# Kernel optimization log

Measured on AMD Instinct MI355X. Metric: run time of the kernel, lower is better.

## Reference

```python
import jax, jax.numpy as jnp
import numpy as np

E = 512        # emb_size
H = 2 * E      # LSTM units
B = 512        # beam/query batch (batched Python-loop states)
K = 32         # padded candidates per state
T = 8          # max_path_length
N_ENT = 50000
N_REL = 5000


def setup_inputs() -> dict:
    key = jax.random.key(0)
    ks = jax.random.split(key, 12)
    f32 = jnp.float32
    ent_emb = jax.random.normal(ks[0], (N_ENT, E), f32) * 0.05
    rel_emb = jax.random.normal(ks[1], (N_REL, E), f32) * 0.05
    relation = jax.random.normal(ks[2], (B, E), f32) * 0.05
    Wx = jax.random.normal(ks[3], (H, 4 * H), f32) * 0.02
    Wh = jax.random.normal(ks[4], (H, 4 * H), f32) * 0.02
    b = jnp.zeros((4 * H,), f32)
    W1 = jax.random.normal(ks[5], (4 * E, 3 * E), f32) * 0.02
    b1 = jnp.zeros((3 * E,), f32)
    W2 = jax.random.normal(ks[6], (3 * E, 2 * E), f32) * 0.02
    b2 = jnp.zeros((2 * E,), f32)
    current_ids = jax.random.randint(ks[7], (T, B), 0, N_ENT)
    prev_rel_ids = jax.random.randint(ks[8], (T, B), 0, N_REL)
    cand_rel_ids = jax.random.randint(ks[9], (T, B, K), 0, N_REL)
    cand_ent_ids = jax.random.randint(ks[10], (T, B, K), 0, N_ENT)
    return {
        "ent_emb": ent_emb, "rel_emb": rel_emb, "relation": relation,
        "Wx": Wx, "Wh": Wh, "b": b,
        "W1": W1, "b1": b1, "W2": W2, "b2": b2,
        "current_ids": current_ids, "prev_rel_ids": prev_rel_ids,
        "cand_rel_ids": cand_rel_ids, "cand_ent_ids": cand_ent_ids,
    }


def reference(ent_emb, rel_emb, relation, Wx, Wh, b, W1, b1, W2, b2,
              current_ids, prev_rel_ids, cand_rel_ids, cand_ent_ids):
    Bh = relation.shape[0]
    units = Wh.shape[0]
    h0 = jnp.zeros((Bh, units), ent_emb.dtype)
    c0 = jnp.zeros((Bh, units), ent_emb.dtype)

    def step(carry, xs):
        h, c = carry
        cur, prl, crel, cent = xs
        # LSTMCell input: concat(prev relation vec, current entity vec)  [B, 2E]
        x = jnp.concatenate([rel_emb[prl], ent_emb[cur]], axis=-1)
        z = x @ Wx + h @ Wh + b                      # [B, 4H], keras gate order i,f,g,o
        i_, f_, g_, o_ = jnp.split(z, 4, axis=-1)
        c = jax.nn.sigmoid(f_) * c + jax.nn.sigmoid(i_) * jnp.tanh(g_)
        h = jax.nn.sigmoid(o_) * jnp.tanh(c)
        # posterior MLP on concat(ent, history, relation)  [B, 4E] -> [B, 2E]
        feat = jax.nn.relu(jnp.concatenate([ent_emb[cur], h, relation], axis=-1) @ W1 + b1)
        feat = jax.nn.relu(feat @ W2 + b2)
        # candidate embeddings: concat(rel vec, to-entity vec)  [B, K, 2E]
        cand = jnp.concatenate([rel_emb[crel], ent_emb[cent]], axis=-1)
        probs = jax.nn.softmax(jnp.einsum('bkd,bd->bk', cand, feat), axis=-1)
        return (h, c), probs

    _, probs = jax.lax.scan(step, (h0, c0),
                            (current_ids, prev_rel_ids, cand_rel_ids, cand_ent_ids))
    return probs  # [T, B, K]
```

## Files before the change

### kernel.cpp

```cpp
#include <hip/hip_runtime.h>
#include <stdint.h>

typedef __attribute__((ext_vector_type(4))) float f32x4;
typedef __attribute__((ext_vector_type(8))) __bf16 bf16x8;
typedef __attribute__((ext_vector_type(8))) unsigned short u16x8;
typedef __attribute__((ext_vector_type(4))) unsigned short u16x4;

typedef const __attribute__((address_space(1))) unsigned int gu32;
typedef __attribute__((address_space(3))) unsigned int lu32;

__device__ __forceinline__ float b2f(unsigned short u) {
  unsigned int x = ((unsigned int)u) << 16;
  float f; __builtin_memcpy(&f, &x, 4); return f;
}
__device__ __forceinline__ unsigned short f2b(float f) {
  unsigned int x; __builtin_memcpy(&x, &f, 4);
  x += 0x7fffu + ((x >> 16) & 1u);
  return (unsigned short)(x >> 16);
}
__device__ __forceinline__ float sigmoidf(float x) {
  return 1.f / (1.f + __expf(-x));
}
__device__ __forceinline__ float tanh_fast(float x) {
  return 1.f - 2.f / (1.f + __expf(2.f * x));
}

__global__ __launch_bounds__(256) void prep1(
    const float* __restrict__ Wx, unsigned short* __restrict__ WxT,
    const float* __restrict__ Wh, unsigned short* __restrict__ WhT,
    const float* __restrict__ W1, unsigned short* __restrict__ W1T,
    const float* __restrict__ W2, unsigned short* __restrict__ W2T,
    const float* __restrict__ ent, const float* __restrict__ rel,
    const float* __restrict__ rln,
    const int* __restrict__ cur, const int* __restrict__ prl,
    unsigned short* __restrict__ Xall, unsigned short* __restrict__ ERall) {
  __shared__ unsigned short tile[64][72];
  const int tid = threadIdx.x;
  int b = blockIdx.x;
  if (b < 3200) {
    const float* in; unsigned short* out; int R, C, bx, by;
    if (b < 1024)      { in = Wx; out = WxT; R = 1024; C = 4096; bx = b & 63; by = b >> 6; }
    else if (b < 2048) { b -= 1024; in = Wh; out = WhT; R = 1024; C = 4096; bx = b & 63; by = b >> 6; }
    else if (b < 2816) { b -= 2048; in = W1; out = W1T; R = 2048; C = 1536; bx = b % 24; by = b / 24; }
    else               { b -= 2816; in = W2; out = W2T; R = 1536; C = 1024; bx = b & 15; by = b >> 4; }
    const int r0 = by * 64, c0 = bx * 64;
    const int r = tid >> 3;
    const int c8 = (tid & 7) * 8;
#pragma unroll
    for (int i = 0; i < 2; i++) {
      const int rr = r + 32*i;
      const float* src = in + (size_t)(r0 + rr) * C + c0 + c8;
      f32x4 a = *(const f32x4*)src;
      f32x4 bb = *(const f32x4*)(src + 4);
      unsigned short tmp[8];
#pragma unroll
      for (int j = 0; j < 4; j++) { tmp[j] = f2b(a[j]); tmp[4+j] = f2b(bb[j]); }
      *(u16x8*)(&tile[rr][c8 ^ (((rr >> 3) & 7) << 3)]) = *(u16x8*)tmp;
    }
    __syncthreads();
    const int rswz = (tid & 7) << 3;
#pragma unroll
    for (int i = 0; i < 2; i++) {
      const int ro = r + 32*i;
      unsigned short tmp[8];
#pragma unroll
      for (int j = 0; j < 8; j++) tmp[j] = tile[c8 + j][ro ^ rswz];
      *(u16x8*)(out + (size_t)(c0 + ro) * R + r0 + c8) = *(u16x8*)tmp;
    }
  } else {
    const int row = b - 3200;
    const int bb = row & 511;
    const int ci = cur[row], ri = prl[row];
    const int half = tid >> 7;
    const int j = tid & 127;
    const float* src;
    if (half == 0) src = (j < 64) ? (rel + (size_t)ri * 512 + j * 8)
                                  : (ent + (size_t)ci * 512 + (j - 64) * 8);
    else           src = (j < 64) ? (ent + (size_t)ci * 512 + j * 8)
                                  : (rln + (size_t)bb * 512 + (j - 64) * 8);
    f32x4 a = *(const f32x4*)src, c = *(const f32x4*)(src + 4);
    unsigned short t[8];
#pragma unroll
    for (int q = 0; q < 4; q++) { t[q] = f2b(a[q]); t[4+q] = f2b(c[q]); }
    unsigned short* dst = (half == 0 ? Xall : ERall) + (size_t)row * 1024 + j * 8;
    *(u16x8*)dst = *(u16x8*)t;
  }
}

__global__ __launch_bounds__(256) void conv_tables(
    const float* __restrict__ ent, unsigned short* __restrict__ entB,
    const float* __restrict__ rel, unsigned short* __restrict__ relB) {
  const long long N0 = 50000LL * 512 / 8, N1 = 5000LL * 512 / 8;
  long long i = (long long)blockIdx.x * 256 + threadIdx.x;
  if (i >= N0 + N1) return;
  const float* in; unsigned short* out;
  if (i < N0) { in = ent; out = entB; }
  else        { in = rel; out = relB; i -= N0; }
  f32x4 a = *(const f32x4*)(in + i * 8);
  f32x4 c = *(const f32x4*)(in + i * 8 + 4);
  unsigned short t[8];
#pragma unroll
  for (int q = 0; q < 4; q++) { t[q] = f2b(a[q]); t[4+q] = f2b(c[q]); }
  *(u16x8*)(out + i * 8) = *(u16x8*)t;
}

template<bool HAS_BIAS, bool DO_RELU, bool PERM_B, bool ASPLIT, bool LSTM0>
__global__ __launch_bounds__(256) void gemm_bf16(
    const unsigned short* __restrict__ A,
    const unsigned short* __restrict__ A2, int lda,
    const unsigned short* __restrict__ BT, int ldb, int K,
    const float* __restrict__ bias,
    unsigned short* __restrict__ Cout, int ldc,
    const float* __restrict__ gbias,
    unsigned short* __restrict__ Hout, float* __restrict__ Cst) {
  __shared__ unsigned short As[128][64];
  __shared__ unsigned short Bs[128][64];
  const int tid = threadIdx.x;
  const int lane = tid & 63;
  const int w = tid >> 6;
  const int wr = w >> 1, wc = w & 1;
  const int m0 = blockIdx.y * 128, n0 = blockIdx.x * 128;
  f32x4 acc[4][4] = {};
  const int srow = lane >> 3;
  const int scol = ((lane & 7) ^ srow) * 8;

  for (int k0 = 0; k0 < K; k0 += 64) {
    const unsigned short* asrc; int ac;
    if (ASPLIT) {
      if (k0 < 512)       { asrc = A;  ac = k0; }
      else if (k0 < 1536) { asrc = A2; ac = k0 - 512; }
      else                { asrc = A;  ac = k0 - 1024; }
    } else { asrc = A; ac = k0; }
#pragma unroll
    for (int i = 0; i < 4; i++) {
      const int c = w * 4 + i;
      const int row = c * 8 + srow;
      __builtin_amdgcn_global_load_lds(
          (gu32*)(asrc + (size_t)(m0 + row) * lda + ac + scol),
          (lu32*)(&As[0][0] + c * 512), 16, 0, 0);
      const int brow = n0 + row;
      const int prow = PERM_B ? (((brow & 3) << 10) + (brow >> 2)) : brow;
      __builtin_amdgcn_global_load_lds(
          (gu32*)(BT + (size_t)prow * ldb + k0 + scol),
          (lu32*)(&Bs[0][0] + c * 512), 16, 0, 0);
    }
    __syncthreads();
#pragma unroll
    for (int ks = 0; ks < 2; ks++) {
      const int kb = ks * 32 + (lane >> 4) * 8;
      const int kswz = kb ^ ((lane & 7) << 3);
      bf16x8 af[4], bfr[4];
#pragma unroll
      for (int m = 0; m < 4; m++)
        af[m] = *reinterpret_cast<const bf16x8*>(&As[wr*64 + m*16 + (lane & 15)][kswz]);
#pragma unroll
      for (int n = 0; n < 4; n++)
        bfr[n] = *reinterpret_cast<const bf16x8*>(&Bs[wc*64 + n*16 + (lane & 15)][kswz]);
#pragma unroll
      for (int m = 0; m < 4; m++)
#pragma unroll
        for (int n = 0; n < 4; n++)
          acc[m][n] = __builtin_amdgcn_mfma_f32_16x16x32_bf16(af[m], bfr[n], acc[m][n], 0, 0, 0);
    }
    __syncthreads();
  }

  const int cn = lane & 15, rb = (lane >> 4) * 4;
  if (LSTM0 && m0 < 512) {
    const int g = lane & 3;
#pragma unroll
    for (int m = 0; m < 4; m++) {
#pragma unroll
      for (int n = 0; n < 4; n++) {
        const int gn = n0 + wc*64 + n*16 + cn;
        const int u = gn >> 2;
        const float gb = gbias[g * 1024 + u];
        const int row0 = m0 + wr*64 + m*16 + rb;
        const float v0 = acc[m][n][0] + gb;
        const float v1 = acc[m][n][1] + gb;
        const float v2 = acc[m][n][2] + gb;
        const float v3 = acc[m][n][3] + gb;
        auto sel = [&](int idx) {
          return idx == 0 ? v0 : idx == 1 ? v1 : idx == 2 ? v2 : v3;
        };
        const float own = sel(g);
        const float r1 = __shfl_xor(sel(g ^ 1), 1);
        const float r2 = __shfl_xor(sel(g ^ 2), 2);
        const float r3 = __shfl_xor(sel(g ^ 3), 3);
        const float zi = g==0 ? own : g==1 ? r1 : g==2 ? r2 : r3;
        const float zg_= g==0 ? r2  : g==1 ? r3 : g==2 ? own: r1;
        const float zo = g==0 ? r3  : g==1 ? r2 : g==2 ? r1 : own;
        const float cnew = sigmoidf(zi) * tanh_fast(zg_);
        const float h = sigmoidf(zo) * tanh_fast(cnew);
        const size_t hidx = (size_t)(row0 + g) * 1024 + u;
        Cst[hidx] = cnew;
        Hout[hidx] = f2b(h);
      }
    }
    return;
  }
#pragma unroll
  for (int m = 0; m < 4; m++) {
#pragma unroll
    for (int n = 0; n < 4; n++) {
      const int gn = n0 + wc*64 + n*16 + cn;
#pragma unroll
      for (int r = 0; r < 4; r++) {
        const int gm = m0 + wr*64 + m*16 + rb + r;
        float v = acc[m][n][r];
        if (HAS_BIAS) v += bias[gn];
        if (DO_RELU)  v = v > 0.f ? v : 0.f;
        Cout[(size_t)gm * ldc + gn] = f2b(v);
      }
    }
  }
}

__global__ __launch_bounds__(512) void zgemm_lstm(
    const unsigned short* __restrict__ A,
    const unsigned short* __restrict__ BT,
    const unsigned short* __restrict__ pre,
    const float* __restrict__ bias,
    unsigned short* __restrict__ Hout,
    float* __restrict__ Cst) {
  __shared__ unsigned short As[2][64][72];
  __shared__ unsigned short Bs[2][128][72];
  __shared__ f32x4 accL[8][256];
  const int tid = threadIdx.x;
  const int lane = tid & 63;
  const int w = tid >> 6;
  const int q = w >> 2;
  const int wq = w & 3;
  const int wr = wq >> 1, wc = wq & 1;
  const int m0 = blockIdx.y * 64, n0 = blockIdx.x * 128;
  f32x4 acc[2][4] = {};
  const int tq = tid & 255;
  const int rs = tq >> 3;
  const int cs = (tq & 7) * 8;

  for (int k0 = 0; k0 < 512; k0 += 64) {
    const int kk = q * 512 + k0;
#pragma unroll
    for (int i = 0; i < 2; i++)
      *(u16x8*)(&As[q][rs + 32*i][cs]) =
          *(const u16x8*)(A + (size_t)(m0 + rs + 32*i) * 1024 + kk + cs);
#pragma unroll
    for (int i = 0; i < 4; i++) {
      const int brow = n0 + rs + 32*i;
      const int prow = ((brow & 3) << 10) + (brow >> 2);
      *(u16x8*)(&Bs[q][rs + 32*i][cs]) =
          *(const u16x8*)(BT + (size_t)prow * 1024 + kk + cs);
    }
    __syncthreads();
#pragma unroll
    for (int ks = 0; ks < 2; ks++) {
      const int kb = ks * 32 + (lane >> 4) * 8;
      bf16x8 af[2], bfr[4];
#pragma unroll
      for (int m = 0; m < 2; m++)
        af[m] = *reinterpret_cast<const bf16x8*>(&As[q][wr*32 + m*16 + (lane & 15)][kb]);
#pragma unroll
      for (int n = 0; n < 4; n++)
        bfr[n] = *reinterpret_cast<const bf16x8*>(&Bs[q][wc*64 + n*16 + (lane & 15)][kb]);
#pragma unroll
      for (int m = 0; m < 2; m++)
#pragma unroll
        for (int n = 0; n < 4; n++)
          acc[m][n] = __builtin_amdgcn_mfma_f32_16x16x32_bf16(af[m], bfr[n], acc[m][n], 0, 0, 0);
    }
    __syncthreads();
  }

  if (q == 1) {
#pragma unroll
    for (int m = 0; m < 2; m++)
#pragma unroll
      for (int n = 0; n < 4; n++)
        accL[m*4 + n][tq] = acc[m][n];
  }
  __syncthreads();
  if (q == 0) {
    const int cn = lane & 15, rb = (lane >> 4) * 4, g = lane & 3;
#pragma unroll
    for (int m = 0; m < 2; m++) {
#pragma unroll
      for (int n = 0; n < 4; n++) {
        const f32x4 s4 = accL[m*4 + n][tq];
        const int gn = n0 + wc*64 + n*16 + cn;
        const int u = gn >> 2;
        const float gb = bias[g * 1024 + u];
        const int row0 = m0 + wr*32 + m*16 + rb;
        const float v0 = acc[m][n][0] + s4[0] + b2f(pre[(size_t)(row0+0) * 4096 + gn]) + gb;
        const float v1 = acc[m][n][1] + s4[1] + b2f(pre[(size_t)(row0+1) * 4096 + gn]) + gb;
        const float v2 = acc[m][n][2] + s4[2] + b2f(pre[(size_t)(row0+2) * 4096 + gn]) + gb;
        const float v3 = acc[m][n][3] + s4[3] + b2f(pre[(size_t)(row0+3) * 4096 + gn]) + gb;
        auto sel = [&](int idx) {
          return idx == 0 ? v0 : idx == 1 ? v1 : idx == 2 ? v2 : v3;
        };
        const float own = sel(g);
        const float r1 = __shfl_xor(sel(g ^ 1), 1);
        const float r2 = __shfl_xor(sel(g ^ 2), 2);
        const float r3 = __shfl_xor(sel(g ^ 3), 3);
        const float zi = g==0 ? own : g==1 ? r1 : g==2 ? r2 : r3;
        const float zf = g==0 ? r1  : g==1 ? own: g==2 ? r3 : r2;
        const float zg_= g==0 ? r2  : g==1 ? r3 : g==2 ? own: r1;
        const float zo = g==0 ? r3  : g==1 ? r2 : g==2 ? r1 : own;
        const size_t hidx = (size_t)(row0 + g) * 1024 + u;
        const float cnew = sigmoidf(zf) * Cst[hidx] + sigmoidf(zi) * tanh_fast(zg_);
        const float h = sigmoidf(zo) * tanh_fast(cnew);
        Cst[hidx] = cnew;
        Hout[hidx] = f2b(h);
      }
    }
  }
}

__global__ __launch_bounds__(256) void score_softmax(
    const unsigned short* __restrict__ F2,
    const unsigned short* __restrict__ relB,
    const unsigned short* __restrict__ entB,
    const int* __restrict__ crel, const int* __restrict__ cent,
    float* __restrict__ outp) {
  const int b = blockIdx.x;
  const int tid = threadIdx.x;
  const int lane = tid & 63, w = tid >> 6;
  __shared__ float feat[1024];
  __shared__ float logits[32];
  {
    u16x4 fv = ((const u16x4*)(F2 + (size_t)b * 1024))[tid];
#pragma unroll
    for (int j = 0; j < 4; j++) feat[tid * 4 + j] = b2f(fv[j]);
  }
  __syncthreads();
  for (int k = w; k < 32; k += 4) {
    const int ri = crel[b * 32 + k], ei = cent[b * 32 + k];
    u16x8 rv = *(const u16x8*)(relB + (size_t)ri * 512 + lane * 8);
    u16x8 ev = *(const u16x8*)(entB + (size_t)ei * 512 + lane * 8);
    float sum = 0.f;
#pragma unroll
    for (int j = 0; j < 8; j++) {
      sum += b2f(rv[j]) * feat[lane * 8 + j];
      sum += b2f(ev[j]) * feat[512 + lane * 8 + j];
    }
#pragma unroll
    for (int off = 32; off; off >>= 1) sum += __shfl_down(sum, off, 64);
    if (lane == 0) logits[k] = sum;
  }
  __syncthreads();
  if (tid < 32) {
    const float l = logits[tid];
    float mx = l;
#pragma unroll
    for (int off = 16; off; off >>= 1) mx = fmaxf(mx, __shfl_xor(mx, off, 32));
    const float p = __expf(l - mx);
    float s = p;
#pragma unroll
    for (int off = 16; off; off >>= 1) s += __shfl_xor(s, off, 32);
    outp[(size_t)b * 32 + tid] = p / s;
  }
}

extern "C" void kernel_launch(void* const* d_in, const int* in_sizes, int n_in,
                              void* d_out, int out_size, void* d_ws, size_t ws_size,
                              hipStream_t stream) {
  const float* ent      = (const float*)d_in[0];
  const float* rel      = (const float*)d_in[1];
  const float* relation = (const float*)d_in[2];
  const float* Wx       = (const float*)d_in[3];
  const float* Wh       = (const float*)d_in[4];
  const float* bvec     = (const float*)d_in[5];
  const float* W1       = (const float*)d_in[6];
  const float* b1       = (const float*)d_in[7];
  const float* W2       = (const float*)d_in[8];
  const float* b2       = (const float*)d_in[9];
  const int* cur  = (const int*)d_in[10];
  const int* prl  = (const int*)d_in[11];
  const int* crel = (const int*)d_in[12];
  const int* cent = (const int*)d_in[13];
  float* out = (float*)d_out;
  (void)in_sizes; (void)n_in; (void)out_size; (void)ws_size;

  char* wsp = (char*)d_ws;
  auto alloc = [&](size_t bytes) { char* p = wsp; wsp += (bytes + 255) & ~(size_t)255; return p; };
  unsigned short* entB = (unsigned short*)alloc((size_t)50000 * 512 * 2);
  unsigned short* relB = (unsigned short*)alloc((size_t)5000 * 512 * 2);
  unsigned short* WxT  = (unsigned short*)alloc((size_t)4096 * 1024 * 2);
  unsigned short* WhT  = (unsigned short*)alloc((size_t)4096 * 1024 * 2);
  unsigned short* W1T  = (unsigned short*)alloc((size_t)1536 * 2048 * 2);
  unsigned short* W2T  = (unsigned short*)alloc((size_t)1024 * 1536 * 2);
  unsigned short* Xall = (unsigned short*)alloc((size_t)4096 * 1024 * 2);
  unsigned short* ERall= (unsigned short*)alloc((size_t)4096 * 1024 * 2);
  unsigned short* P1   = (unsigned short*)alloc((size_t)4096 * 4096 * 2);
  unsigned short* Hall = (unsigned short*)alloc((size_t)4096 * 1024 * 2);
  unsigned short* F1   = (unsigned short*)alloc((size_t)4096 * 1536 * 2);
  unsigned short* F2   = (unsigned short*)alloc((size_t)4096 * 1024 * 2);
  float*          C    = (float*)         alloc((size_t)512 * 1024 * 4);

  const dim3 blk(256);
  const size_t HS = (size_t)512 * 1024;

  prep1<<<7296, blk, 0, stream>>>(
      Wx, WxT, Wh, WhT, W1, W1T, W2, W2T,
      ent, rel, relation, cur, prl, Xall, ERall);

  gemm_bf16<false,false,true,false,true><<<dim3(32, 32), blk, 0, stream>>>(
      Xall, nullptr, 1024, WxT, 1024, 1024, nullptr, P1, 4096, bvec, Hall, C);

  for (int t = 1; t < 8; t++) {
    zgemm_lstm<<<dim3(32, 8), dim3(512), 0, stream>>>(
        Hall + (size_t)(t - 1) * HS, WhT,
        P1 + (size_t)t * 512 * 4096, bvec,
        Hall + (size_t)t * HS, C);
  }

  gemm_bf16<true,true,false,true,false><<<dim3(12, 32), blk, 0, stream>>>(
      ERall, Hall, 1024, W1T, 2048, 2048, b1, F1, 1536, nullptr, nullptr, nullptr);
  gemm_bf16<true,true,false,false,false><<<dim3(8, 32), blk, 0, stream>>>(
      F1, nullptr, 1536, W2T, 1536, 1536, b2, F2, 1024, nullptr, nullptr, nullptr);

  conv_tables<<<13750, blk, 0, stream>>>(ent, entB, rel, relB);
  score_softmax<<<4096, 256, 0, stream>>>(F2, relB, entB, crel, cent, out);
}
```

Measured before the change: 328.5 us.

## Double-buffer LSTM GEMM tiles via async global-to-LDS loads with XOR swizzle

The LSTM gate GEMM kernel now stages A and B tiles straight from global memory into shared memory with global_load_lds, into two buffers, so the next k-tile loads while the current one is multiplied. The padded LDS layout is replaced by an XOR-swizzled 64-column layout to avoid bank conflicts, and register staging copies are removed. This doubles LDS use for the tiles. The loop also drops one barrier per iteration, so correctness depends on the async loads being complete and visible before the next buffer is read.

```diff
diff --git a/kernel.cpp b/kernel.cpp
--- a/kernel.cpp
+++ b/kernel.cpp
@@ -223,8 +223,8 @@
     const float* __restrict__ bias,
     unsigned short* __restrict__ Hout,
     float* __restrict__ Cst) {
-  __shared__ unsigned short As[2][64][72];
-  __shared__ unsigned short Bs[2][128][72];
+  __shared__ unsigned short As[2][2][64][64];
+  __shared__ unsigned short Bs[2][2][128][64];
   __shared__ f32x4 accL[8][256];
   const int tid = threadIdx.x;
   const int lane = tid & 63;
@@ -235,33 +235,47 @@
   const int m0 = blockIdx.y * 64, n0 = blockIdx.x * 128;
   f32x4 acc[2][4] = {};
   const int tq = tid & 255;
-  const int rs = tq >> 3;
-  const int cs = (tq & 7) * 8;
-
+  const int srow = lane >> 3;
+  const int scol = ((lane & 7) ^ srow) * 8;
+
+  auto STAGE = [&](int buf, int k0) {
+    const int kk = q * 512 + k0;
+#pragma unroll
+    for (int i = 0; i < 2; i++) {
+      const int c = wq * 2 + i;
+      const int row = c * 8 + srow;
+      __builtin_amdgcn_global_load_lds(
+          (gu32*)(A + (size_t)(m0 + row) * 1024 + kk + scol),
+          (lu32*)(&As[buf][q][0][0] + c * 512), 16, 0, 0);
+    }
+#pragma unroll
+    for (int i = 0; i < 4; i++) {
+      const int c = wq * 4 + i;
+      const int row = c * 8 + srow;
+      const int brow = n0 + row;
+      const int prow = ((brow & 3) << 10) + (brow >> 2);
+      __builtin_amdgcn_global_load_lds(
+          (gu32*)(BT + (size_t)prow * 1024 + kk + scol),
+          (lu32*)(&Bs[buf][q][0][0] + c * 512), 16, 0, 0);
+    }
+  };
+
+  STAGE(0, 0);
+  __syncthreads();
   for (int k0 = 0; k0 < 512; k0 += 64) {
-    const int kk = q * 512 + k0;
-#pragma unroll
-    for (int i = 0; i < 2; i++)
-      *(u16x8*)(&As[q][rs + 32*i][cs]) =
-          *(const u16x8*)(A + (size_t)(m0 + rs + 32*i) * 1024 + kk + cs);
-#pragma unroll
-    for (int i = 0; i < 4; i++) {
-      const int brow = n0 + rs + 32*i;
-      const int prow = ((brow & 3) << 10) + (brow >> 2);
-      *(u16x8*)(&Bs[q][rs + 32*i][cs]) =
-          *(const u16x8*)(BT + (size_t)prow * 1024 + kk + cs);
-    }
-    __syncthreads();
+    const int buf = (k0 >> 6) & 1;
+    if (k0 + 64 < 512) STAGE(buf ^ 1, k0 + 64);
 #pragma unroll
     for (int ks = 0; ks < 2; ks++) {
       const int kb = ks * 32 + (lane >> 4) * 8;
+      const int kswz = kb ^ ((lane & 7) << 3);
       bf16x8 af[2], bfr[4];
 #pragma unroll
       for (int m = 0; m < 2; m++)
-        af[m] = *reinterpret_cast<const bf16x8*>(&As[q][wr*32 + m*16 + (lane & 15)][kb]);
+        af[m] = *reinterpret_cast<const bf16x8*>(&As[buf][q][wr*32 + m*16 + (lane & 15)][kswz]);
 #pragma unroll
       for (int n = 0; n < 4; n++)
-        bfr[n] = *reinterpret_cast<const bf16x8*>(&Bs[q][wc*64 + n*16 + (lane & 15)][kb]);
+        bfr[n] = *reinterpret_cast<const bf16x8*>(&Bs[buf][q][wc*64 + n*16 + (lane & 15)][kswz]);
 #pragma unroll
       for (int m = 0; m < 2; m++)
 #pragma unroll
```

Result: no change. 322.8 us (-1.8%).
